# Kernel optimization log

Measured on AMD Instinct MI355X. Metric: run time of the kernel, lower is better.

## Reference

```python
import jax, jax.numpy as jnp
import numpy as np

B, S, T = 32, 64, 64
E, H, V = 512, 512, 32000
HD = 2 * H  # decoder hidden size (bidirectional encoder)
NEG = -1e9


def _lstm_cell(x, h, c, Wih, Whh, bih, bhh):
    # torch.nn.LSTMCell gate order: i, f, g, o
    g = x @ Wih.T + bih + h @ Whh.T + bhh
    i, f, gg, o = jnp.split(g, 4, axis=-1)
    c = jax.nn.sigmoid(f) * c + jax.nn.sigmoid(i) * jnp.tanh(gg)
    h = jax.nn.sigmoid(o) * jnp.tanh(c)
    return h, c


def _run_lstm(x, Wih, Whh, bih, bhh, hsz):
    # x: (B, S, E) -> hidden states (B, S, hsz). Faithful to lstm_traverse
    # (zero initial state, forward traversal).
    b = x.shape[0]
    h0 = jnp.zeros((b, hsz), x.dtype)

    def step(carry, xt):
        h, c = _lstm_cell(xt, carry[0], carry[1], Wih, Whh, bih, bhh)
        return (h, c), h

    _, Hs = jax.lax.scan(step, (h0, h0), jnp.swapaxes(x, 0, 1))
    return jnp.swapaxes(Hs, 0, 1)


def setup_inputs() -> dict:
    key = jax.random.key(0)
    ks = jax.random.split(key, 20)
    sc = 0.05
    inp = {
        'src_tokens': jax.random.randint(ks[0], (B, S), 0, V).astype(jnp.int32),
        'src_lens': jax.random.randint(ks[1], (B,), 1, S + 1).astype(jnp.int32),
        'trg_tokens': jax.random.randint(ks[2], (B, T), 0, V).astype(jnp.int32),
        'trg_lens': jax.random.randint(ks[3], (B,), 2, T + 1).astype(jnp.int32),
        'src_emb': jax.random.normal(ks[4], (V, E), jnp.float32) * sc,
        'trg_emb': jax.random.normal(ks[5], (V, E), jnp.float32) * sc,
        # encoder forward cell
        'We_ih': jax.random.normal(ks[6], (4 * H, E), jnp.float32) * sc,
        'We_hh': jax.random.normal(ks[7], (4 * H, H), jnp.float32) * sc,
        'be_ih': jnp.zeros((4 * H,), jnp.float32),
        'be_hh': jnp.zeros((4 * H,), jnp.float32),
        # encoder 'reverse' cell (note: source code traverses forward too)
        'Wr_ih': jax.random.normal(ks[8], (4 * H, E), jnp.float32) * sc,
        'Wr_hh': jax.random.normal(ks[9], (4 * H, H), jnp.float32) * sc,
        'br_ih': jnp.zeros((4 * H,), jnp.float32),
        'br_hh': jnp.zeros((4 * H,), jnp.float32),
        # decoder cell (hidden = 2H)
        'Wd_ih': jax.random.normal(ks[10], (4 * HD, E), jnp.float32) * sc,
        'Wd_hh': jax.random.normal(ks[11], (4 * HD, HD), jnp.float32) * sc,
        'bd_ih': jnp.zeros((4 * HD,), jnp.float32),
        'bd_hh': jnp.zeros((4 * HD,), jnp.float32),
        # output projection: (h, context) -> vocab, in = 4H
        'W_out': jax.random.normal(ks[12], (V, 2 * HD), jnp.float32) * sc,
        'b_out': jnp.zeros((V,), jnp.float32),
    }
    return inp


def _forward(src_tokens, src_lens, trg_tokens, trg_lens,
             src_emb, trg_emb,
             We_ih, We_hh, be_ih, be_hh,
             Wr_ih, Wr_hh, br_ih, br_hh,
             Wd_ih, Wd_hh, bd_ih, bd_hh,
             W_out, b_out):
    # ---- encode ----
    x = src_emb[src_tokens]                                  # (B,S,E)
    Hf = _run_lstm(x, We_ih, We_hh, be_ih, be_hh, H)
    Hr = _run_lstm(x, Wr_ih, Wr_hh, br_ih, br_hh, H)         # forward traversal, as in source
    src_states = jnp.concatenate([Hf, Hr], axis=-1)          # (B,S,2H)
    bidx = jnp.arange(src_states.shape[0])
    final = src_states[bidx, src_lens - 1]                   # (B,2H)

    # ---- decode (teacher forcing, masked-softmax dot attention) ----
    src_mask = jnp.arange(S)[None, :] < src_lens[:, None]    # (B,S)
    h0 = final
    c0 = jnp.zeros_like(final)

    def step(carry, inputs):
        h, c = carry
        tok, tgt = inputs
        v = trg_emb[tok]                                     # (B,E)
        h, c = _lstm_cell(v, h, c, Wd_ih, Wd_hh, bd_ih, bd_hh)
        scores = jnp.einsum('bh,bsh->bs', h, src_states)
        attn = jax.nn.softmax(jnp.where(src_mask, scores, NEG), axis=-1)
        ctx = jnp.einsum('bs,bsh->bh', attn, src_states)     # (B,2H)
        logits = jnp.concatenate([h, ctx], axis=-1) @ W_out.T + b_out
        ls = jax.nn.log_softmax(logits, axis=-1)
        nll = -jnp.take_along_axis(ls, tgt[:, None], axis=-1)[:, 0]
        return (h, c), nll

    in_toks = jnp.swapaxes(trg_tokens[:, :-1], 0, 1)          # (T-1,B)
    tgts = jnp.swapaxes(trg_tokens[:, 1:], 0, 1)              # (T-1,B)
    _, nll = jax.lax.scan(step, (h0, c0), (in_toks, tgts))
    nll = jnp.swapaxes(nll, 0, 1)                             # (B,T-1)

    mask = (jnp.arange(T)[None, :] < trg_lens[:, None]).astype(nll.dtype)
    return jnp.sum(-nll * mask[:, 1:])


def reference(src_tokens, src_lens, trg_tokens, trg_lens,
              src_emb, trg_emb,
              We_ih, We_hh, be_ih, be_hh,
              Wr_ih, Wr_hh, br_ih, br_hh,
              Wd_ih, Wd_hh, bd_ih, bd_hh,
              W_out, b_out):
    return _forward(src_tokens, src_lens, trg_tokens, trg_lens,
                    src_emb, trg_emb,
                    We_ih, We_hh, be_ih, be_hh,
                    Wr_ih, Wr_hh, br_ih, br_hh,
                    Wd_ih, Wd_hh, bd_ih, bd_hh,
                    W_out, b_out)
```

## Files before the change

kernel.cpp:

```cpp
#include <hip/hip_runtime.h>
#include <math.h>

#define NB 32
#define NS 64
#define NT 64
#define NHD 1024
#define NV 32000
#define NR 2016
#define NCT 250
#define RECB 64

typedef unsigned short u16;
typedef __bf16 bf16x8 __attribute__((ext_vector_type(8)));
typedef float f32x4 __attribute__((ext_vector_type(4)));
typedef unsigned u32x4 __attribute__((ext_vector_type(4)));
#define MFMA16 __builtin_amdgcn_mfma_f32_16x16x32_bf16

__device__ __forceinline__ float sigmf(float x) { return 1.f / (1.f + expf(-x)); }
__device__ __forceinline__ u16 f2bf(float f) {
  union { float f; unsigned u; } v; v.f = f;
  unsigned r = v.u + 0x7FFFu + ((v.u >> 16) & 1u);
  return (u16)(r >> 16);
}
__device__ __forceinline__ float bf2f(u16 h) {
  union { unsigned u; float f; } v; v.u = ((unsigned)h) << 16; return v.f;
}

__device__ __forceinline__ u32x4 ldg_coh(const void* p) {
  u32x4 v;
  asm volatile("global_load_dwordx4 %0, %1, off sc0 sc1" : "=v"(v) : "v"(p));
  return v;
}
__device__ __forceinline__ void stg_coh_u32(void* p, unsigned v) {
  asm volatile("global_store_dword %0, %1, off sc0 sc1" :: "v"(p), "v"(v) : "memory");
}
__device__ __forceinline__ unsigned ldg_coh_u32_wait(const void* p) {
  unsigned v;
  asm volatile("global_load_dword %0, %1, off sc0 sc1\n\ts_waitcnt vmcnt(0)"
               : "=v"(v) : "v"(p) : "memory");
  return v;
}
__device__ __forceinline__ void vmwait0() {
  asm volatile("s_waitcnt vmcnt(0)" ::: "memory");
}

__global__ void init_flags_kernel(unsigned* flags) {
  if (threadIdx.x < RECB) flags[threadIdx.x] = 0u;
}

__global__ void rowmap_kernel(const int* __restrict__ trg_lens,
                              unsigned* __restrict__ rowmap, unsigned* __restrict__ mcnt) {
  __shared__ unsigned P[32];
  int tid = threadIdx.x;
  for (int i = tid; i < 2048; i += 256) rowmap[i] = 0u;
  if (tid == 0) {
    unsigned acc = 0;
    for (int b = 0; b < 32; b++) {
      P[b] = acc;
      int L = trg_lens[b]; if (L > NT) L = NT;
      acc += (unsigned)(L - 1);
    }
    mcnt[0] = acc;
  }
  __syncthreads();
  for (int b = 0; b < 32; b++) {
    int L = trg_lens[b]; if (L > NT) L = NT;
    int Lb = L - 1;
    if (tid < Lb) rowmap[P[b] + tid] = (unsigned)(tid * 32 + b);
  }
}

__global__ void gather_src_bf16(const int* tok, const float* emb, u16* out) {
  int idx = blockIdx.x * 256 + threadIdx.x;
  if (idx >= 2048 * 64) return;
  int m = idx >> 6, c8 = (idx & 63) * 8;
  const float4* s = (const float4*)(emb + (size_t)tok[m] * 512 + c8);
  float4 a = s[0], b = s[1];
  union { u16 h[8]; uint4 v; } u;
  u.h[0]=f2bf(a.x); u.h[1]=f2bf(a.y); u.h[2]=f2bf(a.z); u.h[3]=f2bf(a.w);
  u.h[4]=f2bf(b.x); u.h[5]=f2bf(b.y); u.h[6]=f2bf(b.z); u.h[7]=f2bf(b.w);
  *(uint4*)(out + (size_t)m * 512 + c8) = u.v;
}

__global__ void gather_trg_bf16(const int* tok, const float* emb, u16* out) {
  int idx = blockIdx.x * 256 + threadIdx.x;
  if (idx >= NR * 64) return;
  int m = idx >> 6, c8 = (idx & 63) * 8;
  int t = m >> 5, b = m & 31;
  int token = tok[b * NT + t];
  const float4* s = (const float4*)(emb + (size_t)token * 512 + c8);
  float4 a = s[0], bb = s[1];
  union { u16 h[8]; uint4 v; } u;
  u.h[0]=f2bf(a.x); u.h[1]=f2bf(a.y); u.h[2]=f2bf(a.z); u.h[3]=f2bf(a.w);
  u.h[4]=f2bf(bb.x); u.h[5]=f2bf(bb.y); u.h[6]=f2bf(bb.z); u.h[7]=f2bf(bb.w);
  *(uint4*)(out + (size_t)m * 512 + c8) = u.v;
}

__global__ void cvt_bf16_kernel(const float* __restrict__ in, u16* __restrict__ out, long n) {
  long i = ((long)blockIdx.x * 256 + threadIdx.x) * 8;
  if (i >= n) return;
  float4 a = *(const float4*)(in + i);
  float4 b = *(const float4*)(in + i + 4);
  union { u16 h[8]; uint4 v; } u;
  u.h[0]=f2bf(a.x); u.h[1]=f2bf(a.y); u.h[2]=f2bf(a.z); u.h[3]=f2bf(a.w);
  u.h[4]=f2bf(b.x); u.h[5]=f2bf(b.y); u.h[6]=f2bf(b.z); u.h[7]=f2bf(b.w);
  *(uint4*)(out + i) = u.v;
}

__global__ void cvt_dec_frag(const float* __restrict__ W, u16* __restrict__ out) {
  int idx = blockIdx.x * 256 + threadIdx.x;
  if (idx >= 64 * 4 * 32 * 64) return;
  int lane = idx & 63;
  int kk = (idx >> 6) & 31;
  int g = (idx >> 11) & 3;
  int jt = idx >> 13;
  int row = g * 1024 + jt * 16 + (lane & 15);
  int col = kk * 32 + (lane >> 4) * 8;
  const float4* s = (const float4*)(W + (size_t)row * NHD + col);
  float4 a = s[0], b = s[1];
  union { u16 h[8]; uint4 v; } u;
  u.h[0]=f2bf(a.x); u.h[1]=f2bf(a.y); u.h[2]=f2bf(a.z); u.h[3]=f2bf(a.w);
  u.h[4]=f2bf(b.x); u.h[5]=f2bf(b.y); u.h[6]=f2bf(b.z); u.h[7]=f2bf(b.w);
  *(uint4*)(out + (size_t)idx * 8) = u.v;
}

__global__ void cvt_wo_frag(const float* __restrict__ W, u16* __restrict__ out) {
  long idx = (long)blockIdx.x * 256 + threadIdx.x;
  if (idx >= (long)2000 * 64 * 64) return;
  int lane = (int)(idx & 63);
  int kk = (int)((idx >> 6) & 63);
  long j16 = idx >> 12;
  long row = j16 * 16 + (lane & 15);
  int col = kk * 32 + (lane >> 4) * 8;
  const float4* s = (const float4*)(W + (size_t)row * 2048 + col);
  float4 a = s[0], b = s[1];
  union { u16 h[8]; uint4 v; } u;
  u.h[0]=f2bf(a.x); u.h[1]=f2bf(a.y); u.h[2]=f2bf(a.z); u.h[3]=f2bf(a.w);
  u.h[4]=f2bf(b.x); u.h[5]=f2bf(b.y); u.h[6]=f2bf(b.z); u.h[7]=f2bf(b.w);
  *(uint4*)(out + (size_t)idx * 8) = u.v;
}

__global__ void yfrag_repack(const u16* __restrict__ Ybf, const unsigned* __restrict__ rowmap,
                             u16* __restrict__ out) {
  int idx = blockIdx.x * 256 + threadIdx.x;
  if (idx >= 128 * 64 * 64) return;
  int lane = idx & 63;
  int kk = (idx >> 6) & 63;
  int im = idx >> 12;
  int rr = (int)rowmap[im * 16 + (lane & 15)];
  int col = kk * 32 + (lane >> 4) * 8;
  *(uint4*)(out + (size_t)idx * 8) = *(const uint4*)(Ybf + (size_t)rr * 2048 + col);
}

__global__ __launch_bounds__(256) void mfma_gemm_bias(
    const u16* __restrict__ A, const u16* __restrict__ Bm,
    const float* __restrict__ b0, const float* __restrict__ b1,
    float* __restrict__ C, int M, int N, int K) {
  int tid = threadIdx.x, wave = tid >> 6, lane = tid & 63;
  int r = lane & 15, q = lane >> 4;
  int mh = wave >> 1, nh = wave & 1;
  int rowbase = blockIdx.x * 128 + mh * 64;
  int colbase = blockIdx.y * 128 + nh * 64;
  f32x4 acc[4][4] = {};
  for (int k0 = 0; k0 < K; k0 += 32) {
    bf16x8 a[4], b[4];
#pragma unroll
    for (int mt = 0; mt < 4; mt++) {
      int rb = rowbase + mt * 16 + r;
      if (rb >= M) rb = 0;
      a[mt] = *(const bf16x8*)(A + (size_t)rb * K + k0 + q * 8);
    }
#pragma unroll
    for (int nt = 0; nt < 4; nt++)
      b[nt] = *(const bf16x8*)(Bm + (size_t)(colbase + nt * 16 + r) * K + k0 + q * 8);
#pragma unroll
    for (int mt = 0; mt < 4; mt++)
#pragma unroll
      for (int nt = 0; nt < 4; nt++)
        acc[mt][nt] = MFMA16(a[mt], b[nt], acc[mt][nt], 0, 0, 0);
  }
#pragma unroll
  for (int nt = 0; nt < 4; nt++) {
    int gn = colbase + nt * 16 + r;
    float bb = b0[gn] + b1[gn];
#pragma unroll
    for (int mt = 0; mt < 4; mt++)
#pragma unroll
      for (int j = 0; j < 4; j++) {
        int gm = rowbase + mt * 16 + q * 4 + j;
        if (gm < M) C[(size_t)gm * N + gn] = acc[mt][nt][j] + bb;
      }
  }
}

#define ENC_H_OFF 65536
#define ENC_G_OFF 98304
#define DEC_G_OFF 65536
__global__ __launch_bounds__(256, 1) void recurrence_kernel(
    const u16* __restrict__ Wbf_e,
    const u16* __restrict__ Wfragd,
    const float* __restrict__ Aef, const float* __restrict__ Aer, const float* __restrict__ Ad,
    const int* __restrict__ src_lens,
    u16* __restrict__ ssb, float* __restrict__ hs_dec, u16* __restrict__ Ybf,
    u16* __restrict__ hbf_e,
    u16* __restrict__ hbf_d,
    unsigned* flags) {
  __shared__ __align__(16) char smem[107008];
  const int tid = threadIdx.x, bid = blockIdx.x;
  const int wave = tid >> 6, lane = tid & 63;
  const int r = lane & 15, q = lane >> 4;
  const int g = wave;
  const int ob = tid >> 3;
  const int oj = (tid & 7) * 2;
  const int slen_ob = src_lens[ob];
  unsigned tgt = 0;

#define FLAGBAR(fbase, fcnt)                                                        \
  do {                                                                              \
    tgt++;                                                                          \
    vmwait0();                                                                      \
    __syncthreads();                                                                \
    if (wave == 0) {                                                                \
      if (lane == 0) stg_coh_u32(flags + bid, tgt);                                 \
      unsigned fv = tgt;                                                            \
      do {                                                                          \
        if (lane < (fcnt)) fv = ldg_coh_u32_wait(flags + (fbase) + lane);           \
      } while (__any(fv < tgt));                                                    \
    }                                                                               \
    __syncthreads();                                                                \
  } while (0)

  {
    const int lstm = bid >> 5, jt = bid & 31;
    float* gates = (float*)(smem + ENC_G_OFF);
    for (int c = tid; c < 64 * 64; c += 256) {
      int lr = c >> 6, c8 = (c & 63) * 8;
      int grow = lstm * 2048 + (lr >> 4) * 512 + jt * 16 + (lr & 15);
      uint4 v = *(const uint4*)(Wbf_e + (size_t)grow * 512 + c8);
      *(uint4*)(smem + ((lr * 1024 + c8 * 2) ^ ((lr & 7) << 4))) = v;
    }
    const float* Ae = lstm ? Aer : Aef;
    const int jcol = jt * 16 + oj;
    float creg0 = 0.f, creg1 = 0.f;
    for (int t = 0; t < NS; t++) {
      size_t abase = ((size_t)ob * NS + t) * 2048;
      float2 vi = *(const float2*)(Ae + abase + jcol);
      float2 vf = *(const float2*)(Ae + abase + 512 + jcol);
      float2 vg = *(const float2*)(Ae + abase + 1024 + jcol);
      float2 vo = *(const float2*)(Ae + abase + 1536 + jcol);
      if (t == 0) {
        u32x4 z = {0u, 0u, 0u, 0u};
#pragma unroll
        for (int k = 0; k < 8; k++) {
          int c = tid + k * 256;
          int hr = c >> 6, seg = c & 63;
          *(u32x4*)(smem + (ENC_H_OFF + ((hr * 1024 + seg * 16) ^ ((hr & 7) << 4)))) = z;
        }
      } else {
        const u16* hsrc = hbf_e + ((size_t)(t & 1) * 2 + lstm) * 16384;
        u32x4 hv[8];
#pragma unroll
        for (int k = 0; k < 8; k++) hv[k] = ldg_coh(hsrc + (tid + k * 256) * 8);
        vmwait0();
#pragma unroll
        for (int k = 0; k < 8; k++) {
          int c = tid + k * 256;
          int hr = c >> 6, seg = c & 63;
          *(u32x4*)(smem + (ENC_H_OFF + ((hr * 1024 + seg * 16) ^ ((hr & 7) << 4)))) = hv[k];
        }
      }
      __syncthreads();
      f32x4 acc0 = {0.f,0.f,0.f,0.f}, acc1 = {0.f,0.f,0.f,0.f};
      for (int ks = 0; ks < 512; ks += 32) {
        int col2 = (ks + q * 8) * 2;
        int a0r = r, a1r = 16 + r, br = g * 16 + r;
        bf16x8 a0 = *(const bf16x8*)(smem + (ENC_H_OFF + ((a0r * 1024 + col2) ^ ((a0r & 7) << 4))));
        bf16x8 a1 = *(const bf16x8*)(smem + (ENC_H_OFF + ((a1r * 1024 + col2) ^ ((a1r & 7) << 4))));
        bf16x8 bf = *(const bf16x8*)(smem + ((br * 1024 + col2) ^ ((br & 7) << 4)));
        acc0 = MFMA16(a0, bf, acc0, 0, 0, 0);
        acc1 = MFMA16(a1, bf, acc1, 0, 0, 0);
      }
#pragma unroll
      for (int j = 0; j < 4; j++) {
        gates[(g * 32 + q * 4 + j) * 17 + r] = acc0[j];
        gates[(g * 32 + 16 + q * 4 + j) * 17 + r] = acc1[j];
      }
      __syncthreads();
      {
        float I0 = vi.x + gates[(0 * 32 + ob) * 17 + oj];
        float I1 = vi.y + gates[(0 * 32 + ob) * 17 + oj + 1];
        float F0 = vf.x + gates[(1 * 32 + ob) * 17 + oj];
        float F1 = vf.y + gates[(1 * 32 + ob) * 17 + oj + 1];
        float G0 = vg.x + gates[(2 * 32 + ob) * 17 + oj];
        float G1 = vg.y + gates[(2 * 32 + ob) * 17 + oj + 1];
        float O0 = vo.x + gates[(3 * 32 + ob) * 17 + oj];
        float O1 = vo.y + gates[(3 * 32 + ob) * 17 + oj + 1];
        float c0 = sigmf(F0) * creg0 + sigmf(I0) * tanhf(G0);
        float c1 = sigmf(F1) * creg1 + sigmf(I1) * tanhf(G1);
        float h0 = sigmf(O0) * tanhf(c0);
        float h1 = sigmf(O1) * tanhf(c1);
        creg0 = c0; creg1 = c1;
        unsigned hv2 = ((unsigned)f2bf(h1) << 16) | f2bf(h0);
        stg_coh_u32(hbf_e + ((size_t)((t + 1) & 1) * 2 + lstm) * 16384 + ob * 512 + jcol, hv2);
        *(unsigned*)(ssb + ((size_t)ob * NS + t) * NHD + lstm * 512 + jcol) = hv2;
        if (t == slen_ob - 1)
          stg_coh_u32(hbf_d + ob * NHD + lstm * 512 + jcol, hv2);
      }
      FLAGBAR(lstm * 32, 32);
    }
  }

  FLAGBAR(0, RECB);

  {
    const int jt = bid;
    const int jcol = jt * 16 + oj;
    float* gates = (float*)(smem + DEC_G_OFF);
    const u16* wbase = Wfragd + (size_t)(jt * 4 + g) * 16384;
    float cd0 = 0.f, cd1 = 0.f;
    for (int t = 0; t < NT - 1; t++) {
      const float* ad = Ad + ((size_t)t * NB + ob) * 4096;
      float2 vi = *(const float2*)(ad + jcol);
      float2 vf = *(const float2*)(ad + 1024 + jcol);
      float2 vg = *(const float2*)(ad + 2048 + jcol);
      float2 vo = *(const float2*)(ad + 3072 + jcol);
      const u16* hsrc = hbf_d + (size_t)(t & 1) * (32 * NHD);
      {
        u32x4 hv[16];
#pragma unroll
        for (int k = 0; k < 16; k++) hv[k] = ldg_coh(hsrc + (tid + k * 256) * 8);
        vmwait0();
#pragma unroll
        for (int k = 0; k < 16; k++) {
          int c = tid + k * 256;
          int hr = c >> 7, seg = c & 127;
          *(u32x4*)(smem + ((hr * 2048 + seg * 16) ^ ((hr & 7) << 4))) = hv[k];
        }
      }
      __syncthreads();
      f32x4 acc0 = {0.f,0.f,0.f,0.f}, acc1 = {0.f,0.f,0.f,0.f};
      for (int kk = 0; kk < 32; kk++) {
        int colb = (kk * 32 + q * 8) * 2;
        int a0r = r, a1r = 16 + r;
        bf16x8 a0 = *(const bf16x8*)(smem + ((a0r * 2048 + colb) ^ ((a0r & 7) << 4)));
        bf16x8 a1 = *(const bf16x8*)(smem + ((a1r * 2048 + colb) ^ ((a1r & 7) << 4)));
        bf16x8 bf = *(const bf16x8*)(wbase + ((size_t)kk * 64 + lane) * 8);
        acc0 = MFMA16(a0, bf, acc0, 0, 0, 0);
        acc1 = MFMA16(a1, bf, acc1, 0, 0, 0);
      }
#pragma unroll
      for (int j = 0; j < 4; j++) {
        gates[(g * 32 + q * 4 + j) * 17 + r] = acc0[j];
        gates[(g * 32 + 16 + q * 4 + j) * 17 + r] = acc1[j];
      }
      __syncthreads();
      {
        float I0 = vi.x + gates[(0 * 32 + ob) * 17 + oj];
        float I1 = vi.y + gates[(0 * 32 + ob) * 17 + oj + 1];
        float F0 = vf.x + gates[(1 * 32 + ob) * 17 + oj];
        float F1 = vf.y + gates[(1 * 32 + ob) * 17 + oj + 1];
        float G0 = vg.x + gates[(2 * 32 + ob) * 17 + oj];
        float G1 = vg.y + gates[(2 * 32 + ob) * 17 + oj + 1];
        float O0 = vo.x + gates[(3 * 32 + ob) * 17 + oj];
        float O1 = vo.y + gates[(3 * 32 + ob) * 17 + oj + 1];
        float c0 = sigmf(F0) * cd0 + sigmf(I0) * tanhf(G0);
        float c1 = sigmf(F1) * cd1 + sigmf(I1) * tanhf(G1);
        float h0 = sigmf(O0) * tanhf(c0);
        float h1 = sigmf(O1) * tanhf(c1);
        cd0 = c0; cd1 = c1;
        size_t rowY = (size_t)t * NB + ob;
        unsigned hv2 = ((unsigned)f2bf(h1) << 16) | f2bf(h0);
        stg_coh_u32(hbf_d + (size_t)((t + 1) & 1) * (32 * NHD) + ob * NHD + jcol, hv2);
        *(unsigned*)(Ybf + rowY * 2048 + jcol) = hv2;
        float2 hvf; hvf.x = h0; hvf.y = h1;
        *(float2*)(hs_dec + rowY * NHD + jcol) = hvf;
      }
      if (t != NT - 2) FLAGBAR(0, RECB);
    }
  }
#undef FLAGBAR
}

__global__ __launch_bounds__(256) void attn_kernel(const float* __restrict__ hs,
                                                   const u16* __restrict__ ssb,
                                                   const int* __restrict__ src_lens,
                                                   const unsigned* __restrict__ rowmap,
                                                   const unsigned* __restrict__ mcnt,
                                                   u16* __restrict__ Ybf) {
  __shared__ __align__(16) float hsh[NHD];
  __shared__ float sc[NS];
  __shared__ float att[NS];
  int cr = blockIdx.x;
  if ((unsigned)cr >= mcnt[0]) return;
  int rr = (int)rowmap[cr];
  int b = rr & 31;
  int tid = threadIdx.x;
  for (int i = tid; i < NHD; i += 256) hsh[i] = hs[(size_t)rr * NHD + i];
  __syncthreads();
  {
    int s = tid >> 2, q = tid & 3;
    const u16* row = ssb + ((size_t)b * NS + s) * NHD + q * 256;
    const float* h4 = hsh + q * 256;
    float p = 0.f;
    for (int k = 0; k < 256; k += 8) {
      uint4 v = *(const uint4*)(row + k);
      p += h4[k + 0] * bf2f((u16)(v.x & 0xFFFF)) + h4[k + 1] * bf2f((u16)(v.x >> 16));
      p += h4[k + 2] * bf2f((u16)(v.y & 0xFFFF)) + h4[k + 3] * bf2f((u16)(v.y >> 16));
      p += h4[k + 4] * bf2f((u16)(v.z & 0xFFFF)) + h4[k + 5] * bf2f((u16)(v.z >> 16));
      p += h4[k + 6] * bf2f((u16)(v.w & 0xFFFF)) + h4[k + 7] * bf2f((u16)(v.w >> 16));
    }
    p += __shfl_xor(p, 1);
    p += __shfl_xor(p, 2);
    if (q == 0) sc[s] = (s < src_lens[b]) ? p : -1e9f;
  }
  __syncthreads();
  if (tid < 64) {
    float v = sc[tid];
    float m = v;
#pragma unroll
    for (int off = 1; off < 64; off <<= 1) m = fmaxf(m, __shfl_xor(m, off));
    float e = expf(v - m);
    float ssum = e;
#pragma unroll
    for (int off = 1; off < 64; off <<= 1) ssum += __shfl_xor(ssum, off);
    att[tid] = e / ssum;
  }
  __syncthreads();
  float a0 = 0, a1 = 0, a2 = 0, a3 = 0;
  int d = tid * 4;
  for (int s2 = 0; s2 < NS; s2++) {
    float a = att[s2];
    uint2 v = *(const uint2*)(ssb + ((size_t)b * NS + s2) * NHD + d);
    a0 += a * bf2f((u16)(v.x & 0xFFFF));
    a1 += a * bf2f((u16)(v.x >> 16));
    a2 += a * bf2f((u16)(v.y & 0xFFFF));
    a3 += a * bf2f((u16)(v.y >> 16));
  }
  ushort4 o;
  o.x = f2bf(a0); o.y = f2bf(a1); o.z = f2bf(a2); o.w = f2bf(a3);
  *(ushort4*)(Ybf + (size_t)rr * 2048 + NHD + d) = o;
}

__global__ __launch_bounds__(256) void gemmlse_mfma(
    const u16* __restrict__ Yf,
    const u16* __restrict__ Wf,
    const float* __restrict__ bo, const int* __restrict__ trg_tok,
    const unsigned* __restrict__ rowmap, const unsigned* __restrict__ mcnt,
    float* __restrict__ pm, float* __restrict__ ps, float* __restrict__ tgtlog) {
  __shared__ int tgtc[128];
  __shared__ float pmp[2][128];
  __shared__ float psp[2][128];
  int o = blockIdx.x;
  int u = (o & 7) * 500 + (o >> 3);
  int bm = u & 15, bn = u >> 4;
  const int M = (int)mcnt[0];
  if (bm * 128 >= M) return;
  int tid = threadIdx.x;
  int wave = tid >> 6, lane = tid & 63;
  int r = lane & 15, q = lane >> 4;
  int mh = wave >> 1, nh = wave & 1;
  if (tid < 128) {
    int gm = bm * 128 + tid;
    if (gm < M) {
      int rr = (int)rowmap[gm];
      int tt = rr >> 5, b = rr & 31;
      tgtc[tid] = trg_tok[b * NT + tt + 1];
    } else {
      tgtc[tid] = -1;
    }
  }
  __syncthreads();
  const u16* ybase = Yf + (((size_t)(bm * 8 + mh * 4) * 64) * 64 + lane) * 8;
  const u16* wbase = Wf + (((size_t)(bn * 8 + nh * 4) * 64) * 64 + lane) * 8;
  f32x4 acc[4][4] = {};
  for (int kk = 0; kk < 64; kk += 2) {
    bf16x8 aA[4], bA[4], aB[4], bB[4];
#pragma unroll
    for (int mt = 0; mt < 4; mt++) {
      const u16* p = ybase + ((size_t)mt * 64 + kk) * 512;
      aA[mt] = *(const bf16x8*)(p);
      aB[mt] = *(const bf16x8*)(p + 512);
    }
#pragma unroll
    for (int nt = 0; nt < 4; nt++) {
      const u16* p = wbase + ((size_t)nt * 64 + kk) * 512;
      bA[nt] = *(const bf16x8*)(p);
      bB[nt] = *(const bf16x8*)(p + 512);
    }
#pragma unroll
    for (int mt = 0; mt < 4; mt++)
#pragma unroll
      for (int nt = 0; nt < 4; nt++)
        acc[mt][nt] = MFMA16(aA[mt], bA[nt], acc[mt][nt], 0, 0, 0);
#pragma unroll
    for (int mt = 0; mt < 4; mt++)
#pragma unroll
      for (int nt = 0; nt < 4; nt++)
        acc[mt][nt] = MFMA16(aB[mt], bB[nt], acc[mt][nt], 0, 0, 0);
  }
  int colbase = bn * 128 + nh * 64;
  float bo4[4];
#pragma unroll
  for (int nt = 0; nt < 4; nt++) bo4[nt] = bo[colbase + nt * 16 + r];
#pragma unroll
  for (int mt = 0; mt < 4; mt++)
#pragma unroll
    for (int nt = 0; nt < 4; nt++)
#pragma unroll
      for (int j = 0; j < 4; j++) acc[mt][nt][j] += bo4[nt];
#pragma unroll
  for (int mt = 0; mt < 4; mt++) {
#pragma unroll
    for (int j = 0; j < 4; j++) {
      float m = fmaxf(fmaxf(acc[mt][0][j], acc[mt][1][j]), fmaxf(acc[mt][2][j], acc[mt][3][j]));
      m = fmaxf(m, __shfl_xor(m, 1));
      m = fmaxf(m, __shfl_xor(m, 2));
      m = fmaxf(m, __shfl_xor(m, 4));
      m = fmaxf(m, __shfl_xor(m, 8));
      float s = expf(acc[mt][0][j] - m) + expf(acc[mt][1][j] - m) +
                expf(acc[mt][2][j] - m) + expf(acc[mt][3][j] - m);
      s += __shfl_xor(s, 1);
      s += __shfl_xor(s, 2);
      s += __shfl_xor(s, 4);
      s += __shfl_xor(s, 8);
      int lrow = mh * 64 + mt * 16 + q * 4 + j;
      if (r == 0) { pmp[nh][lrow] = m; psp[nh][lrow] = s; }
      int tc = tgtc[lrow];
      int off = tc - (bn * 128 + nh * 64);
      if (off >= 0 && off < 64 && (off & 15) == r) {
        tgtlog[bm * 128 + lrow] = acc[mt][off >> 4][j];
      }
    }
  }
  __syncthreads();
  if (tid < 128) {
    int gm = bm * 128 + tid;
    if (gm < M) {
      float m0 = pmp[0][tid], m1 = pmp[1][tid];
      float m = fmaxf(m0, m1);
      float s = psp[0][tid] * expf(m0 - m) + psp[1][tid] * expf(m1 - m);
      pm[(size_t)bn * NR + gm] = m;
      ps[(size_t)bn * NR + gm] = s;
    }
  }
}

__global__ void lse_combine_kernel(const float* __restrict__ pm, const float* __restrict__ ps,
                                   const float* __restrict__ tgtlog,
                                   const unsigned* __restrict__ mcnt,
                                   float* __restrict__ rowval) {
  int cr = blockIdx.x * blockDim.x + threadIdx.x;
  if (cr >= NR) return;
  if ((unsigned)cr >= mcnt[0]) { rowval[cr] = 0.f; return; }
  float m = -1e30f;
  for (int i = 0; i < NCT; i++) m = fmaxf(m, pm[(size_t)i * NR + cr]);
  float s = 0.f;
  for (int i = 0; i < NCT; i++) s += ps[(size_t)i * NR + cr] * expf(pm[(size_t)i * NR + cr] - m);
  float lse = m + logf(s);
  rowval[cr] = tgtlog[cr] - lse;
}

__global__ void final_reduce_kernel(const float* __restrict__ rowval, float* __restrict__ out) {
  __shared__ float sm[256];
  float s = 0.f;
  for (int i = threadIdx.x; i < NR; i += 256) s += rowval[i];
  sm[threadIdx.x] = s;
  __syncthreads();
  for (int off = 128; off > 0; off >>= 1) {
    if (threadIdx.x < off) sm[threadIdx.x] += sm[threadIdx.x + off];
    __syncthreads();
  }
  if (threadIdx.x == 0) out[0] = sm[0];
}

extern "C" void kernel_launch(void* const* d_in, const int* in_sizes, int n_in,
                              void* d_out, int out_size, void* d_ws, size_t ws_size,
                              hipStream_t stream) {
  const int* src_tokens = (const int*)d_in[0];
  const int* src_lens = (const int*)d_in[1];
  const int* trg_tokens = (const int*)d_in[2];
  const int* trg_lens = (const int*)d_in[3];
  const float* src_emb = (const float*)d_in[4];
  const float* trg_emb = (const float*)d_in[5];
  const float* We_ih = (const float*)d_in[6];
  const float* We_hh = (const float*)d_in[7];
  const float* be_ih = (const float*)d_in[8];
  const float* be_hh = (const float*)d_in[9];
  const float* Wr_ih = (const float*)d_in[10];
  const float* Wr_hh = (const float*)d_in[11];
  const float* br_ih = (const float*)d_in[12];
  const float* br_hh = (const float*)d_in[13];
  const float* Wd_ih = (const float*)d_in[14];
  const float* Wd_hh = (const float*)d_in[15];
  const float* bd_ih = (const float*)d_in[16];
  const float* bd_hh = (const float*)d_in[17];
  const float* W_out = (const float*)d_in[18];
  const float* b_out = (const float*)d_in[19];

  char* base = (char*)d_ws;
  size_t off = 0;
  auto alloc = [&](size_t bytes) -> char* {
    char* p = base + off;
    off += (bytes + 255) & ~(size_t)255;
    return p;
  };
  u16* xsrcb = (u16*)alloc((size_t)2048 * 512 * 2);
  u16* xtrgb = (u16*)alloc((size_t)NR * 512 * 2);
  u16* Wihe = (u16*)alloc((size_t)2048 * 512 * 2);
  u16* Wihr = (u16*)alloc((size_t)2048 * 512 * 2);
  u16* Wihd = (u16*)alloc((size_t)4096 * 512 * 2);
  u16* Wbf_e = (u16*)alloc((size_t)4096 * 512 * 2);
  u16* Wfragd = (u16*)alloc((size_t)4096 * 1024 * 2);
  u16* Wofrag = (u16*)alloc((size_t)NV * 2048 * 2);
  u16* Yfrag = (u16*)alloc((size_t)128 * 64 * 64 * 8 * 2);
  float* Aef = (float*)alloc((size_t)2048 * 2048 * 4);
  float* Aer = (float*)alloc((size_t)2048 * 2048 * 4);
  float* Ad  = (float*)alloc((size_t)NR * 4096 * 4);
  u16* ssb  = (u16*)alloc((size_t)NB * NS * NHD * 2);
  float* hs_dec = (float*)alloc((size_t)NR * NHD * 4);
  u16* Ybf = (u16*)alloc((size_t)NR * 2048 * 2);
  u16* hbf_e = (u16*)alloc((size_t)4 * 32 * 512 * 2);
  u16* hbf_d = (u16*)alloc((size_t)2 * 32 * NHD * 2);
  float* pm = (float*)alloc((size_t)NCT * NR * 4);
  float* ps = (float*)alloc((size_t)NCT * NR * 4);
  float* tgtlog = (float*)alloc((size_t)NR * 4);
  float* rowval = (float*)alloc((size_t)NR * 4);
  unsigned* flags = (unsigned*)alloc(256);
  unsigned* rowmap = (unsigned*)alloc(2048 * 4);
  unsigned* mcnt = (unsigned*)alloc(256);

  init_flags_kernel<<<1, 64, 0, stream>>>(flags);
  rowmap_kernel<<<1, 256, 0, stream>>>(trg_lens, rowmap, mcnt);

  gather_src_bf16<<<512, 256, 0, stream>>>(src_tokens, src_emb, xsrcb);
  gather_trg_bf16<<<(NR * 64 + 255) / 256, 256, 0, stream>>>(trg_tokens, trg_emb, xtrgb);

  cvt_bf16_kernel<<<512, 256, 0, stream>>>(We_ih, Wihe, (long)2048 * 512);
  cvt_bf16_kernel<<<512, 256, 0, stream>>>(Wr_ih, Wihr, (long)2048 * 512);
  cvt_bf16_kernel<<<1024, 256, 0, stream>>>(Wd_ih, Wihd, (long)4096 * 512);
  cvt_bf16_kernel<<<512, 256, 0, stream>>>(We_hh, Wbf_e, (long)2048 * 512);
  cvt_bf16_kernel<<<512, 256, 0, stream>>>(Wr_hh, Wbf_e + (size_t)2048 * 512, (long)2048 * 512);
  cvt_dec_frag<<<2048, 256, 0, stream>>>(Wd_hh, Wfragd);
  cvt_wo_frag<<<32000, 256, 0, stream>>>(W_out, Wofrag);

  mfma_gemm_bias<<<dim3(16, 16), 256, 0, stream>>>(xsrcb, Wihe, be_ih, be_hh, Aef, 2048, 2048, 512);
  mfma_gemm_bias<<<dim3(16, 16), 256, 0, stream>>>(xsrcb, Wihr, br_ih, br_hh, Aer, 2048, 2048, 512);
  mfma_gemm_bias<<<dim3(16, 32), 256, 0, stream>>>(xtrgb, Wihd, bd_ih, bd_hh, Ad, NR, 4096, 512);

  recurrence_kernel<<<RECB, 256, 0, stream>>>(Wbf_e, Wfragd, Aef, Aer, Ad, src_lens,
                                              ssb, hs_dec, Ybf, hbf_e, hbf_d, flags);

  attn_kernel<<<NR, 256, 0, stream>>>(hs_dec, ssb, src_lens, rowmap, mcnt, Ybf);

  yfrag_repack<<<2048, 256, 0, stream>>>(Ybf, rowmap, Yfrag);

  gemmlse_mfma<<<4000, 256, 0, stream>>>(Yfrag, Wofrag, b_out, trg_tokens, rowmap, mcnt, pm, ps, tgtlog);
  lse_combine_kernel<<<(NR + 255) / 256, 256, 0, stream>>>(pm, ps, tgtlog, mcnt, rowval);
  final_reduce_kernel<<<1, 256, 0, stream>>>(rowval, (float*)d_out);
}
```

Baseline: 1.294 ms.

## Merge prep kernels, batch input GEMMs, and move W_out conversion into attention

Fuses the many small prep launches (flag init, rowmap, embedding gathers, weight conversions) into one block-indexed prep kernel. The three input-projection GEMMs become a single launch split by blockIdx.y. The large W_out bf16 fragment conversion is moved out of the prologue into extra blocks of the attention kernel, where it runs alongside attention work after the recurrence. This removes launch overhead and gaps between kernels. The cost is a longer attention kernel, with 128 blocks each looping over 64000 elements.

Result: slower. 1.408 ms (+8.8%).

```diff
diff --git a/kernel.cpp b/kernel.cpp
--- a/kernel.cpp
+++ b/kernel.cpp
@@ -44,61 +44,7 @@
   asm volatile("s_waitcnt vmcnt(0)" ::: "memory");
 }
 
-__global__ void init_flags_kernel(unsigned* flags) {
-  if (threadIdx.x < RECB) flags[threadIdx.x] = 0u;
-}
-
-__global__ void rowmap_kernel(const int* __restrict__ trg_lens,
-                              unsigned* __restrict__ rowmap, unsigned* __restrict__ mcnt) {
-  __shared__ unsigned P[32];
-  int tid = threadIdx.x;
-  for (int i = tid; i < 2048; i += 256) rowmap[i] = 0u;
-  if (tid == 0) {
-    unsigned acc = 0;
-    for (int b = 0; b < 32; b++) {
-      P[b] = acc;
-      int L = trg_lens[b]; if (L > NT) L = NT;
-      acc += (unsigned)(L - 1);
-    }
-    mcnt[0] = acc;
-  }
-  __syncthreads();
-  for (int b = 0; b < 32; b++) {
-    int L = trg_lens[b]; if (L > NT) L = NT;
-    int Lb = L - 1;
-    if (tid < Lb) rowmap[P[b] + tid] = (unsigned)(tid * 32 + b);
-  }
-}
-
-__global__ void gather_src_bf16(const int* tok, const float* emb, u16* out) {
-  int idx = blockIdx.x * 256 + threadIdx.x;
-  if (idx >= 2048 * 64) return;
-  int m = idx >> 6, c8 = (idx & 63) * 8;
-  const float4* s = (const float4*)(emb + (size_t)tok[m] * 512 + c8);
-  float4 a = s[0], b = s[1];
-  union { u16 h[8]; uint4 v; } u;
-  u.h[0]=f2bf(a.x); u.h[1]=f2bf(a.y); u.h[2]=f2bf(a.z); u.h[3]=f2bf(a.w);
-  u.h[4]=f2bf(b.x); u.h[5]=f2bf(b.y); u.h[6]=f2bf(b.z); u.h[7]=f2bf(b.w);
-  *(uint4*)(out + (size_t)m * 512 + c8) = u.v;
-}
-
-__global__ void gather_trg_bf16(const int* tok, const float* emb, u16* out) {
-  int idx = blockIdx.x * 256 + threadIdx.x;
-  if (idx >= NR * 64) return;
-  int m = idx >> 6, c8 = (idx & 63) * 8;
-  int t = m >> 5, b = m & 31;
-  int token = tok[b * NT + t];
-  const float4* s = (const float4*)(emb + (size_t)token * 512 + c8);
-  float4 a = s[0], bb = s[1];
-  union { u16 h[8]; uint4 v; } u;
-  u.h[0]=f2bf(a.x); u.h[1]=f2bf(a.y); u.h[2]=f2bf(a.z); u.h[3]=f2bf(a.w);
-  u.h[4]=f2bf(bb.x); u.h[5]=f2bf(bb.y); u.h[6]=f2bf(bb.z); u.h[7]=f2bf(bb.w);
-  *(uint4*)(out + (size_t)m * 512 + c8) = u.v;
-}
-
-__global__ void cvt_bf16_kernel(const float* __restrict__ in, u16* __restrict__ out, long n) {
-  long i = ((long)blockIdx.x * 256 + threadIdx.x) * 8;
-  if (i >= n) return;
+__device__ __forceinline__ void cvt8(const float* __restrict__ in, u16* __restrict__ out, long i) {
   float4 a = *(const float4*)(in + i);
   float4 b = *(const float4*)(in + i + 4);
   union { u16 h[8]; uint4 v; } u;
@@ -107,72 +53,114 @@
   *(uint4*)(out + i) = u.v;
 }
 
-__global__ void cvt_dec_frag(const float* __restrict__ W, u16* __restrict__ out) {
-  int idx = blockIdx.x * 256 + threadIdx.x;
-  if (idx >= 64 * 4 * 32 * 64) return;
-  int lane = idx & 63;
-  int kk = (idx >> 6) & 31;
-  int g = (idx >> 11) & 3;
-  int jt = idx >> 13;
-  int row = g * 1024 + jt * 16 + (lane & 15);
-  int col = kk * 32 + (lane >> 4) * 8;
-  const float4* s = (const float4*)(W + (size_t)row * NHD + col);
-  float4 a = s[0], b = s[1];
-  union { u16 h[8]; uint4 v; } u;
-  u.h[0]=f2bf(a.x); u.h[1]=f2bf(a.y); u.h[2]=f2bf(a.z); u.h[3]=f2bf(a.w);
-  u.h[4]=f2bf(b.x); u.h[5]=f2bf(b.y); u.h[6]=f2bf(b.z); u.h[7]=f2bf(b.w);
-  *(uint4*)(out + (size_t)idx * 8) = u.v;
-}
-
-__global__ void cvt_wo_frag(const float* __restrict__ W, u16* __restrict__ out) {
-  long idx = (long)blockIdx.x * 256 + threadIdx.x;
-  if (idx >= (long)2000 * 64 * 64) return;
-  int lane = (int)(idx & 63);
-  int kk = (int)((idx >> 6) & 63);
-  long j16 = idx >> 12;
-  long row = j16 * 16 + (lane & 15);
-  int col = kk * 32 + (lane >> 4) * 8;
-  const float4* s = (const float4*)(W + (size_t)row * 2048 + col);
-  float4 a = s[0], b = s[1];
-  union { u16 h[8]; uint4 v; } u;
-  u.h[0]=f2bf(a.x); u.h[1]=f2bf(a.y); u.h[2]=f2bf(a.z); u.h[3]=f2bf(a.w);
-  u.h[4]=f2bf(b.x); u.h[5]=f2bf(b.y); u.h[6]=f2bf(b.z); u.h[7]=f2bf(b.w);
-  *(uint4*)(out + (size_t)idx * 8) = u.v;
-}
-
-__global__ void yfrag_repack(const u16* __restrict__ Ybf, const unsigned* __restrict__ rowmap,
-                             u16* __restrict__ out) {
-  int idx = blockIdx.x * 256 + threadIdx.x;
-  if (idx >= 128 * 64 * 64) return;
-  int lane = idx & 63;
-  int kk = (idx >> 6) & 63;
-  int im = idx >> 12;
-  int rr = (int)rowmap[im * 16 + (lane & 15)];
-  int col = kk * 32 + (lane >> 4) * 8;
-  *(uint4*)(out + (size_t)idx * 8) = *(const uint4*)(Ybf + (size_t)rr * 2048 + col);
-}
-
-__global__ __launch_bounds__(256) void mfma_gemm_bias(
-    const u16* __restrict__ A, const u16* __restrict__ Bm,
-    const float* __restrict__ b0, const float* __restrict__ b1,
-    float* __restrict__ C, int M, int N, int K) {
+__global__ __launch_bounds__(256) void prep_kernel(
+    const int* __restrict__ src_tokens, const int* __restrict__ trg_tokens,
+    const int* __restrict__ trg_lens,
+    const float* __restrict__ src_emb, const float* __restrict__ trg_emb,
+    const float* __restrict__ We_ih, const float* __restrict__ Wr_ih,
+    const float* __restrict__ Wd_ih, const float* __restrict__ We_hh,
+    const float* __restrict__ Wr_hh, const float* __restrict__ Wd_hh,
+    u16* __restrict__ xsrcb, u16* __restrict__ xtrgb,
+    u16* __restrict__ Wihe, u16* __restrict__ Wihr, u16* __restrict__ Wihd,
+    u16* __restrict__ Wbf_e, u16* __restrict__ Wfragd,
+    unsigned* __restrict__ rowmap, unsigned* __restrict__ mcnt, unsigned* __restrict__ flags) {
+  int b = blockIdx.x, tid = threadIdx.x;
+  if (b < 512) {
+    int idx = b * 256 + tid;
+    int m = idx >> 6, c8 = (idx & 63) * 8;
+    const float4* s = (const float4*)(src_emb + (size_t)src_tokens[m] * 512 + c8);
+    float4 a = s[0], bb = s[1];
+    union { u16 h[8]; uint4 v; } u;
+    u.h[0]=f2bf(a.x); u.h[1]=f2bf(a.y); u.h[2]=f2bf(a.z); u.h[3]=f2bf(a.w);
+    u.h[4]=f2bf(bb.x); u.h[5]=f2bf(bb.y); u.h[6]=f2bf(bb.z); u.h[7]=f2bf(bb.w);
+    *(uint4*)(xsrcb + (size_t)m * 512 + c8) = u.v;
+  } else if (b < 1016) {
+    int idx = (b - 512) * 256 + tid;
+    int m = idx >> 6, c8 = (idx & 63) * 8;
+    int t = m >> 5, bb2 = m & 31;
+    int token = trg_tokens[bb2 * NT + t];
+    const float4* s = (const float4*)(trg_emb + (size_t)token * 512 + c8);
+    float4 a = s[0], bb = s[1];
+    union { u16 h[8]; uint4 v; } u;
+    u.h[0]=f2bf(a.x); u.h[1]=f2bf(a.y); u.h[2]=f2bf(a.z); u.h[3]=f2bf(a.w);
+    u.h[4]=f2bf(bb.x); u.h[5]=f2bf(bb.y); u.h[6]=f2bf(bb.z); u.h[7]=f2bf(bb.w);
+    *(uint4*)(xtrgb + (size_t)m * 512 + c8) = u.v;
+  } else if (b < 1528) {
+    cvt8(We_ih, Wihe, ((long)(b - 1016) * 256 + tid) * 8);
+  } else if (b < 2040) {
+    cvt8(Wr_ih, Wihr, ((long)(b - 1528) * 256 + tid) * 8);
+  } else if (b < 3064) {
+    cvt8(Wd_ih, Wihd, ((long)(b - 2040) * 256 + tid) * 8);
+  } else if (b < 3576) {
+    cvt8(We_hh, Wbf_e, ((long)(b - 3064) * 256 + tid) * 8);
+  } else if (b < 4088) {
+    cvt8(Wr_hh, Wbf_e + (size_t)2048 * 512, ((long)(b - 3576) * 256 + tid) * 8);
+  } else if (b < 6136) {
+    int idx = (b - 4088) * 256 + tid;
+    int lane = idx & 63;
+    int kk = (idx >> 6) & 31;
+    int g = (idx >> 11) & 3;
+    int jt = idx >> 13;
+    int row = g * 1024 + jt * 16 + (lane & 15);
+    int col = kk * 32 + (lane >> 4) * 8;
+    const float4* s = (const float4*)(Wd_hh + (size_t)row * NHD + col);
+    float4 a = s[0], bb = s[1];
+    union { u16 h[8]; uint4 v; } u;
+    u.h[0]=f2bf(a.x); u.h[1]=f2bf(a.y); u.h[2]=f2bf(a.z); u.h[3]=f2bf(a.w);
+    u.h[4]=f2bf(bb.x); u.h[5]=f2bf(bb.y); u.h[6]=f2bf(bb.z); u.h[7]=f2bf(bb.w);
+    *(uint4*)(Wfragd + (size_t)idx * 8) = u.v;
+  } else if (b == 6136) {
+    __shared__ unsigned P[32];
+    for (int i = tid; i < 2048; i += 256) rowmap[i] = 0u;
+    if (tid == 0) {
+      unsigned acc = 0;
+      for (int bb2 = 0; bb2 < 32; bb2++) {
+        P[bb2] = acc;
+        int L = trg_lens[bb2]; if (L > NT) L = NT;
+        acc += (unsigned)(L - 1);
+      }
+      mcnt[0] = acc;
+    }
+    __syncthreads();
+    for (int bb2 = 0; bb2 < 32; bb2++) {
+      int L = trg_lens[bb2]; if (L > NT) L = NT;
+      int Lb = L - 1;
+      if (tid < Lb) rowmap[P[bb2] + tid] = (unsigned)(tid * 32 + bb2);
+    }
+  } else {
+    flags[tid] = 0u;
+  }
+}
+
+__global__ __launch_bounds__(256) void mfma_gemm3(
+    const u16* __restrict__ xsrcb, const u16* __restrict__ xtrgb,
+    const u16* __restrict__ Wihe, const u16* __restrict__ Wihr, const u16* __restrict__ Wihd,
+    const float* __restrict__ be_ih, const float* __restrict__ be_hh,
+    const float* __restrict__ br_ih, const float* __restrict__ br_hh,
+    const float* __restrict__ bd_ih, const float* __restrict__ bd_hh,
+    float* __restrict__ Aef, float* __restrict__ Aer, float* __restrict__ Ad) {
+  int by = blockIdx.y;
+  const u16 *A, *Bm; const float *b0, *b1; float* C; int M, N, colTile;
+  if (by < 16)      { A = xsrcb; Bm = Wihe; b0 = be_ih; b1 = be_hh; C = Aef; M = 2048; N = 2048; colTile = by; }
+  else if (by < 32) { A = xsrcb; Bm = Wihr; b0 = br_ih; b1 = br_hh; C = Aer; M = 2048; N = 2048; colTile = by - 16; }
+  else              { A = xtrgb; Bm = Wihd; b0 = bd_ih; b1 = bd_hh; C = Ad;  M = NR;   N = 4096; colTile = by - 32; }
   int tid = threadIdx.x, wave = tid >> 6, lane = tid & 63;
   int r = lane & 15, q = lane >> 4;
   int mh = wave >> 1, nh = wave & 1;
   int rowbase = blockIdx.x * 128 + mh * 64;
-  int colbase = blockIdx.y * 128 + nh * 64;
+  int colbase = colTile * 128 + nh * 64;
   f32x4 acc[4][4] = {};
-  for (int k0 = 0; k0 < K; k0 += 32) {
+  for (int k0 = 0; k0 < 512; k0 += 32) {
     bf16x8 a[4], b[4];
 #pragma unroll
     for (int mt = 0; mt < 4; mt++) {
       int rb = rowbase + mt * 16 + r;
       if (rb >= M) rb = 0;
-      a[mt] = *(const bf16x8*)(A + (size_t)rb * K + k0 + q * 8);
+      a[mt] = *(const bf16x8*)(A + (size_t)rb * 512 + k0 + q * 8);
     }
 #pragma unroll
     for (int nt = 0; nt < 4; nt++)
-      b[nt] = *(const bf16x8*)(Bm + (size_t)(colbase + nt * 16 + r) * K + k0 + q * 8);
+      b[nt] = *(const bf16x8*)(Bm + (size_t)(colbase + nt * 16 + r) * 512 + k0 + q * 8);
 #pragma unroll
     for (int mt = 0; mt < 4; mt++)
 #pragma unroll
@@ -386,15 +374,34 @@
                                                    const int* __restrict__ src_lens,
                                                    const unsigned* __restrict__ rowmap,
                                                    const unsigned* __restrict__ mcnt,
+                                                   const float* __restrict__ W_out,
+                                                   u16* __restrict__ Wofrag,
                                                    u16* __restrict__ Ybf) {
   __shared__ __align__(16) float hsh[NHD];
   __shared__ float sc[NS];
   __shared__ float att[NS];
+  int tid = threadIdx.x;
+  if (blockIdx.x >= NR) {
+    long c0 = (long)(blockIdx.x - NR) * 64000;
+    for (long idx = c0 + tid; idx < c0 + 64000; idx += 256) {
+      int lane2 = (int)(idx & 63);
+      int kk = (int)((idx >> 6) & 63);
+      long j16 = idx >> 12;
+      long row = j16 * 16 + (lane2 & 15);
+      int col = kk * 32 + (lane2 >> 4) * 8;
+      const float4* s = (const float4*)(W_out + (size_t)row * 2048 + col);
+      float4 a = s[0], b = s[1];
+      union { u16 h[8]; uint4 v; } u;
+      u.h[0]=f2bf(a.x); u.h[1]=f2bf(a.y); u.h[2]=f2bf(a.z); u.h[3]=f2bf(a.w);
+      u.h[4]=f2bf(b.x); u.h[5]=f2bf(b.y); u.h[6]=f2bf(b.z); u.h[7]=f2bf(b.w);
+      *(uint4*)(Wofrag + (size_t)idx * 8) = u.v;
+    }
+    return;
+  }
   int cr = blockIdx.x;
   if ((unsigned)cr >= mcnt[0]) return;
   int rr = (int)rowmap[cr];
   int b = rr & 31;
-  int tid = threadIdx.x;
   for (int i = tid; i < NHD; i += 256) hsh[i] = hs[(size_t)rr * NHD + i];
   __syncthreads();
   {
@@ -439,6 +446,18 @@
   ushort4 o;
   o.x = f2bf(a0); o.y = f2bf(a1); o.z = f2bf(a2); o.w = f2bf(a3);
   *(ushort4*)(Ybf + (size_t)rr * 2048 + NHD + d) = o;
+}
+
+__global__ void yfrag_repack(const u16* __restrict__ Ybf, const unsigned* __restrict__ rowmap,
+                             u16* __restrict__ out) {
+  int idx = blockIdx.x * 256 + threadIdx.x;
+  if (idx >= 128 * 64 * 64) return;
+  int lane = idx & 63;
+  int kk = (idx >> 6) & 63;
+  int im = idx >> 12;
+  int rr = (int)rowmap[im * 16 + (lane & 15)];
+  int col = kk * 32 + (lane >> 4) * 8;
+  *(uint4*)(out + (size_t)idx * 8) = *(const uint4*)(Ybf + (size_t)rr * 2048 + col);
 }
 
 __global__ __launch_bounds__(256) void gemmlse_mfma(
@@ -625,32 +644,24 @@
   float* ps = (float*)alloc((size_t)NCT * NR * 4);
   float* tgtlog = (float*)alloc((size_t)NR * 4);
   float* rowval = (float*)alloc((size_t)NR * 4);
-  unsigned* flags = (unsigned*)alloc(256);
+  unsigned* flags = (unsigned*)alloc(1024);
   unsigned* rowmap = (unsigned*)alloc(2048 * 4);
   unsigned* mcnt = (unsigned*)alloc(256);
 
-  init_flags_kernel<<<1, 64, 0, stream>>>(flags);
-  rowmap_kernel<<<1, 256, 0, stream>>>(trg_lens, rowmap, mcnt);
-
-  gather_src_bf16<<<512, 256, 0, stream>>>(src_tokens, src_emb, xsrcb);
-  gather_trg_bf16<<<(NR * 64 + 255) / 256, 256, 0, stream>>>(trg_tokens, trg_emb, xtrgb);
-
-  cvt_bf16_kernel<<<512, 256, 0, stream>>>(We_ih, Wihe, (long)2048 * 512);
-  cvt_bf16_kernel<<<512, 256, 0, stream>>>(Wr_ih, Wihr, (long)2048 * 512);
-  cvt_bf16_kernel<<<1024, 256, 0, stream>>>(Wd_ih, Wihd, (long)4096 * 512);
-  cvt_bf16_kernel<<<512, 256, 0, stream>>>(We_hh, Wbf_e, (long)2048 * 512);
-  cvt_bf16_kernel<<<512, 256, 0, stream>>>(Wr_hh, Wbf_e + (size_t)2048 * 512, (long)2048 * 512);
-  cvt_dec_frag<<<2048, 256, 0, stream>>>(Wd_hh, Wfragd);
-  cvt_wo_frag<<<32000, 256, 0, stream>>>(W_out, Wofrag);
-
-  mfma_gemm_bias<<<dim3(16, 16), 256, 0, stream>>>(xsrcb, Wihe, be_ih, be_hh, Aef, 2048, 2048, 512);
-  mfma_gemm_bias<<<dim3(16, 16), 256, 0, stream>>>(xsrcb, Wihr, br_ih, br_hh, Aer, 2048, 2048, 512);
-  mfma_gemm_bias<<<dim3(16, 32), 256, 0, stream>>>(xtrgb, Wihd, bd_ih, bd_hh, Ad, NR, 4096, 512);
+  prep_kernel<<<6138, 256, 0, stream>>>(
+      src_tokens, trg_tokens, trg_lens, src_emb, trg_emb,
+      We_ih, Wr_ih, Wd_ih, We_hh, Wr_hh, Wd_hh,
+      xsrcb, xtrgb, Wihe, Wihr, Wihd, Wbf_e, Wfragd, rowmap, mcnt, flags);
+
+  mfma_gemm3<<<dim3(16, 64), 256, 0, stream>>>(
+      xsrcb, xtrgb, Wihe, Wihr, Wihd,
+      be_ih, be_hh, br_ih, br_hh, bd_ih, bd_hh, Aef, Aer, Ad);
 
   recurrence_kernel<<<RECB, 256, 0, stream>>>(Wbf_e, Wfragd, Aef, Aer, Ad, src_lens,
                                               ssb, hs_dec, Ybf, hbf_e, hbf_d, flags);
 
-  attn_kernel<<<NR, 256, 0, stream>>>(hs_dec, ssb, src_lens, rowmap, mcnt, Ybf);
+  attn_kernel<<<NR + 128, 256, 0, stream>>>(hs_dec, ssb, src_lens, rowmap, mcnt,
+                                            W_out, Wofrag, Ybf);
 
   yfrag_repack<<<2048, 256, 0, stream>>>(Ybf, rowmap, Yfrag);
 
```
